# Performance work log

Measured on AMD Instinct MI355X. Metric: run time of the kernel, lower is better.

The kernel has to match this reference:

```python
import jax, jax.numpy as jnp
import numpy as np

N = 50000      # nodes
E = 320000     # edges
D_NODE = 256   # node feature size
D_EDGE = 128   # raw edge feature size
T_DIM = 64     # time encoder out_channels
H = 8          # heads (auto_num_heads(256) -> 8)
C = 32         # per-head dim = 256 // 8
D_E_IN = D_EDGE + T_DIM  # edge_dim into lin_edge


def setup_inputs() -> dict:
    key = jax.random.key(0)
    ks = jax.random.split(key, 16)
    s_n = 1.0 / np.sqrt(D_NODE)
    s_e = 1.0 / np.sqrt(D_E_IN)
    return {
        "edge_tuples": jax.random.randint(ks[0], (2, E), 0, N, dtype=jnp.int64)
        if jax.config.jax_enable_x64 else jax.random.randint(ks[0], (2, E), 0, N),
        "edge_feats": jax.random.normal(ks[1], (E, D_EDGE), jnp.float32),
        "edge_times_rel": jax.random.uniform(ks[2], (E,), jnp.float32) * 100.0,
        "node_feats": jax.random.normal(ks[3], (N, D_NODE), jnp.float32),
        # time encoder: Linear(1, T_DIM) followed by cos
        "w_time": jax.random.normal(ks[4], (T_DIM,), jnp.float32),
        "b_time": jax.random.normal(ks[5], (T_DIM,), jnp.float32),
        # TransformerConv linears (out = H*C = 256)
        "Wq": jax.random.normal(ks[6], (H * C, D_NODE), jnp.float32) * s_n,
        "bq": jnp.zeros((H * C,), jnp.float32),
        "Wk": jax.random.normal(ks[7], (H * C, D_NODE), jnp.float32) * s_n,
        "bk": jnp.zeros((H * C,), jnp.float32),
        "Wv": jax.random.normal(ks[8], (H * C, D_NODE), jnp.float32) * s_n,
        "bv": jnp.zeros((H * C,), jnp.float32),
        "We": jax.random.normal(ks[9], (H * C, D_E_IN), jnp.float32) * s_e,  # lin_edge, no bias
        "Ws": jax.random.normal(ks[10], (H * C, D_NODE), jnp.float32) * s_n,  # lin_skip
        "bs": jnp.zeros((H * C,), jnp.float32),
    }


def reference(edge_tuples, edge_feats, edge_times_rel, node_feats,
              w_time, b_time, Wq, bq, Wk, bk, Wv, bv, We, Ws, bs):
    n_nodes = node_feats.shape[0]
    n_edges = edge_tuples.shape[1]
    src, dst = edge_tuples[0], edge_tuples[1]

    # TGN time encoder: cos(t * w + b)  -> [E, T_DIM]
    tfeat = jnp.cos(edge_times_rel[:, None] * w_time[None, :] + b_time)
    e_attr = jnp.concatenate([tfeat, edge_feats], axis=1)  # [E, T_DIM + D_EDGE]

    # dense per-node projections, then gather per edge
    q = (node_feats @ Wq.T + bq)[dst].reshape(n_edges, H, C)
    k = (node_feats @ Wk.T + bk)[src].reshape(n_edges, H, C)
    v = (node_feats @ Wv.T + bv)[src].reshape(n_edges, H, C)
    ep = (e_attr @ We.T).reshape(n_edges, H, C)

    k = k + ep
    alpha = jnp.sum(q * k, axis=-1) / jnp.sqrt(jnp.asarray(C, q.dtype))  # [E, H]

    # segment softmax over edges grouped by destination node
    m = jax.ops.segment_max(alpha, dst, num_segments=n_nodes)  # [N, H]
    m = jnp.where(jnp.isfinite(m), m, 0.0)
    ea = jnp.exp(alpha - m[dst])
    denom = jax.ops.segment_sum(ea, dst, num_segments=n_nodes)
    a = ea / (denom[dst] + 1e-16)  # [E, H]

    # weighted scatter-aggregate of (value + edge) messages
    msg = a[:, :, None] * (v + ep)  # [E, H, C]
    out = jax.ops.segment_sum(msg, dst, num_segments=n_nodes).reshape(n_nodes, H * C)

    # root / skip connection
    out = out + node_feats @ Ws.T + bs
    return out
```

## Files before the change

kernel.cpp:

```cpp
#include <hip/hip_runtime.h>
#include <hip/hip_bf16.h>
#include <math.h>

#define NN 50000
#define NE 320000
#define SCAN_NBLK ((NN + 255) / 256)

typedef __attribute__((ext_vector_type(8))) short bf16x8;
typedef __attribute__((ext_vector_type(4))) float floatx4;
typedef __attribute__((ext_vector_type(4))) unsigned int uintx4;

static __device__ __forceinline__ unsigned pack2bf(float a, float b) {
    __hip_bfloat162 h = __float22bfloat162_rn(make_float2(a, b));
    return *reinterpret_cast<unsigned*>(&h);
}
static __device__ __forceinline__ unsigned short f2bf(float x) {
    __hip_bfloat16 h = __float2bfloat16(x);
    return *reinterpret_cast<unsigned short*>(&h);
}
static __device__ __forceinline__ float bf2f(unsigned short u) {
    return __uint_as_float(((unsigned)u) << 16);
}
static __device__ __forceinline__ float bflo(unsigned u) {
    return __uint_as_float(u << 16);
}
static __device__ __forceinline__ float bfhi(unsigned u) {
    return __uint_as_float(u & 0xffff0000u);
}
static __device__ __forceinline__ void gload_lds16(const void* g, void* l) {
    __builtin_amdgcn_global_load_lds(
        (const __attribute__((address_space(1))) void*)g,
        (__attribute__((address_space(3))) void*)l, 16, 0, 0);
}

__global__ __launch_bounds__(256)
void cvt_bf16_kernel(const float* __restrict__ in,
                     unsigned short* __restrict__ out, int n8)
{
    int t = blockIdx.x * 256 + threadIdx.x;
    if (t >= n8) return;
    const float4* p = (const float4*)in + (size_t)t * 2;
    float4 a = p[0], b = p[1];
    uint4 u;
    u.x = pack2bf(a.x, a.y); u.y = pack2bf(a.z, a.w);
    u.z = pack2bf(b.x, b.y); u.w = pack2bf(b.z, b.w);
    ((uint4*)out)[t] = u;
}

__global__ __launch_bounds__(256)
void node_gemm_kernel(const unsigned short* __restrict__ Xb,
                      const unsigned short* __restrict__ Wqb,
                      const unsigned short* __restrict__ Wkb,
                      const unsigned short* __restrict__ Wvb,
                      const unsigned short* __restrict__ Wsb,
                      const float* __restrict__ bq, const float* __restrict__ bk,
                      const float* __restrict__ bv, const float* __restrict__ bs,
                      unsigned short* __restrict__ qb,
                      unsigned short* __restrict__ kb,
                      unsigned short* __restrict__ vb,
                      float* __restrict__ outS)
{
    const int m0  = blockIdx.x * 128;
    const int ct  = blockIdx.y;
    const int mat = ct >> 1, half = ct & 1;
    const int colbase = half * 128;

    const unsigned short* __restrict__ W;
    const float* __restrict__ bias;
    switch (mat) {
        case 0:  W = Wqb; bias = bq; break;
        case 1:  W = Wkb; bias = bk; break;
        case 2:  W = Wvb; bias = bv; break;
        default: W = Wsb; bias = bs; break;
    }
    W += (size_t)colbase * 256;

    __shared__ __align__(16) unsigned char smem[32768];
    short* sA = (short*)smem;
    short* sB = (short*)(smem + 16384);

    const int tid  = threadIdx.x;
    const int lane = tid & 63;
    const int wave = tid >> 6;
    const int wm   = (wave & 1) * 64;
    const int wn   = (wave >> 1) * 64;
    const int lr   = lane & 15;
    const int lq   = lane >> 4;

    const int srow = tid >> 3;
    const int scol = (tid & 7) * 8;

    floatx4 acc[4][4];
    #pragma unroll
    for (int i = 0; i < 4; ++i)
        #pragma unroll
        for (int j = 0; j < 4; ++j)
            acc[i][j] = (floatx4){0.f, 0.f, 0.f, 0.f};

    for (int k0 = 0; k0 < 256; k0 += 64) {
        #pragma unroll
        for (int p = 0; p < 4; ++p) {
            int arow = m0 + p * 32 + srow;
            if (arow > NN - 1) arow = NN - 1;
            gload_lds16(Xb + (size_t)arow * 256 + k0 + scol,
                        (char*)sA + p * 4096 + wave * 1024);
            gload_lds16(W + (size_t)(p * 32 + srow) * 256 + k0 + scol,
                        (char*)sB + p * 4096 + wave * 1024);
        }
        __syncthreads();

        #pragma unroll
        for (int ks = 0; ks < 2; ++ks) {
            bf16x8 af[4], bfr[4];
            #pragma unroll
            for (int i = 0; i < 4; ++i)
                af[i] = *(const bf16x8*)&sA[(wm + i * 16 + lr) * 64 + ks * 32 + lq * 8];
            #pragma unroll
            for (int j = 0; j < 4; ++j)
                bfr[j] = *(const bf16x8*)&sB[(wn + j * 16 + lr) * 64 + ks * 32 + lq * 8];
            #pragma unroll
            for (int i = 0; i < 4; ++i)
                #pragma unroll
                for (int j = 0; j < 4; ++j)
                    acc[i][j] = __builtin_amdgcn_mfma_f32_16x16x32_bf16(
                        af[i], bfr[j], acc[i][j], 0, 0, 0);
        }
        __syncthreads();
    }

    if (mat < 3) {
        unsigned short* __restrict__ Cb = (mat == 0) ? qb : (mat == 1) ? kb : vb;
        unsigned short* sOut = (unsigned short*)smem;
        for (int ch = 0; ch < 4; ++ch) {
            __syncthreads();
            if ((ch >> 1) == (wave & 1)) {
                int ibase = (ch & 1) * 2;
                #pragma unroll
                for (int ii = 0; ii < 2; ++ii) {
                    int i = ibase + ii;
                    #pragma unroll
                    for (int j = 0; j < 4; ++j) {
                        int col = wn + j * 16 + lr;
                        float bb = bias[colbase + col];
                        #pragma unroll
                        for (int r = 0; r < 4; ++r) {
                            int rowc = ii * 16 + lq * 4 + r;
                            sOut[rowc * 136 + col] = f2bf(acc[i][j][r] + bb);
                        }
                    }
                }
            }
            __syncthreads();
            #pragma unroll
            for (int p = 0; p < 2; ++p) {
                int rowc = p * 16 + (tid >> 4);
                int off  = (tid & 15) * 8;
                int grow = m0 + ch * 32 + rowc;
                if (grow < NN) {
                    uint4 u = *(const uint4*)&sOut[rowc * 136 + off];
                    *(uint4*)&Cb[(size_t)grow * 256 + colbase + off] = u;
                }
            }
        }
    } else {
        float* sOutF = (float*)smem;
        for (int ch = 0; ch < 8; ++ch) {
            __syncthreads();
            if ((ch >> 2) == (wave & 1)) {
                int i = ch & 3;
                #pragma unroll
                for (int j = 0; j < 4; ++j) {
                    int col = wn + j * 16 + lr;
                    float bb = bias[colbase + col];
                    #pragma unroll
                    for (int r = 0; r < 4; ++r) {
                        int rowc = lq * 4 + r;
                        sOutF[rowc * 132 + col] = acc[i][j][r] + bb;
                    }
                }
            }
            __syncthreads();
            #pragma unroll
            for (int p = 0; p < 2; ++p) {
                int rowc = p * 8 + (tid >> 5);
                int off  = (tid & 31) * 4;
                int grow = m0 + ch * 16 + rowc;
                if (grow < NN) {
                    float4 f = *(const float4*)&sOutF[rowc * 132 + off];
                    *(float4*)&outS[(size_t)grow * 256 + colbase + off] = f;
                }
            }
        }
    }
}

__global__ __launch_bounds__(512)
void edge_gemm_kernel(const float* __restrict__ tvals,
                      const float* __restrict__ w_time,
                      const float* __restrict__ b_time,
                      const float* __restrict__ ef,
                      const unsigned short* __restrict__ Web,
                      unsigned short* __restrict__ epb)
{
    const int m0 = blockIdx.x * 128;

    __shared__ __align__(16) unsigned char smem[49152];
    short* sA = (short*)smem;
    short* sB = (short*)(smem + 16384);

    const int tid  = threadIdx.x;
    const int lane = tid & 63;
    const int wave = tid >> 6;
    const int wm   = (wave & 1) * 64;
    const int wn   = (wave >> 1) * 64;
    const int lr   = lane & 15;
    const int lq   = lane >> 4;

    floatx4 acc[4][4];
    #pragma unroll
    for (int i = 0; i < 4; ++i)
        #pragma unroll
        for (int j = 0; j < 4; ++j)
            acc[i][j] = (floatx4){0.f, 0.f, 0.f, 0.f};

    for (int k0 = 0; k0 < 192; k0 += 64) {
        #pragma unroll
        for (int p = 0; p < 4; ++p)
            gload_lds16(Web + (size_t)(p * 64 + (tid >> 3)) * 192 + k0 + (tid & 7) * 8,
                        (char*)sB + p * 8192 + wave * 1024);

        if (k0 == 0) {
            #pragma unroll
            for (int p = 0; p < 2; ++p) {
                int   row = p * 64 + (tid >> 3);
                float tvv = tvals[m0 + row];
                int   c0  = (tid & 7) * 8;
                float4 w0 = *(const float4*)(w_time + c0);
                float4 w1 = *(const float4*)(w_time + c0 + 4);
                float4 b0 = *(const float4*)(b_time + c0);
                float4 b1 = *(const float4*)(b_time + c0 + 4);
                uint4 u;
                u.x = pack2bf(cosf(fmaf(tvv, w0.x, b0.x)), cosf(fmaf(tvv, w0.y, b0.y)));
                u.y = pack2bf(cosf(fmaf(tvv, w0.z, b0.z)), cosf(fmaf(tvv, w0.w, b0.w)));
                u.z = pack2bf(cosf(fmaf(tvv, w1.x, b1.x)), cosf(fmaf(tvv, w1.y, b1.y)));
                u.w = pack2bf(cosf(fmaf(tvv, w1.z, b1.z)), cosf(fmaf(tvv, w1.w, b1.w)));
                *(uint4*)&sA[p * 4096 + tid * 8] = u;
            }
        } else {
            float4 f[4];
            #pragma unroll
            for (int p = 0; p < 2; ++p) {
                const float4* src = (const float4*)(ef
                    + (size_t)(m0 + p * 64 + (tid >> 3)) * 128 + (k0 - 64) + (tid & 7) * 8);
                f[2 * p]     = src[0];
                f[2 * p + 1] = src[1];
            }
            #pragma unroll
            for (int p = 0; p < 2; ++p) {
                uint4 u;
                u.x = pack2bf(f[2 * p].x,     f[2 * p].y);
                u.y = pack2bf(f[2 * p].z,     f[2 * p].w);
                u.z = pack2bf(f[2 * p + 1].x, f[2 * p + 1].y);
                u.w = pack2bf(f[2 * p + 1].z, f[2 * p + 1].w);
                *(uint4*)&sA[p * 4096 + tid * 8] = u;
            }
        }
        __syncthreads();

        #pragma unroll
        for (int ks = 0; ks < 2; ++ks) {
            bf16x8 af[4], bfr[4];
            #pragma unroll
            for (int i = 0; i < 4; ++i)
                af[i] = *(const bf16x8*)&sA[(wm + i * 16 + lr) * 64 + ks * 32 + lq * 8];
            #pragma unroll
            for (int j = 0; j < 4; ++j)
                bfr[j] = *(const bf16x8*)&sB[(wn + j * 16 + lr) * 64 + ks * 32 + lq * 8];
            #pragma unroll
            for (int i = 0; i < 4; ++i)
                #pragma unroll
                for (int j = 0; j < 4; ++j)
                    acc[i][j] = __builtin_amdgcn_mfma_f32_16x16x32_bf16(
                        af[i], bfr[j], acc[i][j], 0, 0, 0);
        }
        __syncthreads();
    }

    unsigned short* sOut = (unsigned short*)smem;
    for (int ch = 0; ch < 4; ++ch) {
        __syncthreads();
        if ((wave & 1) == (ch >> 1)) {
            int ibase = (ch & 1) * 2;
            #pragma unroll
            for (int ii = 0; ii < 2; ++ii) {
                int i = ibase + ii;
                #pragma unroll
                for (int j = 0; j < 4; ++j) {
                    int col = wn + j * 16 + lr;
                    #pragma unroll
                    for (int r = 0; r < 4; ++r) {
                        int rowc = ii * 16 + lq * 4 + r;
                        sOut[rowc * 264 + col] = f2bf(acc[i][j][r]);
                    }
                }
            }
        }
        __syncthreads();
        #pragma unroll
        for (int p = 0; p < 2; ++p) {
            int rl   = p * 16 + (tid >> 5);
            int off  = (tid & 31) * 8;
            int grow = m0 + ch * 32 + rl;
            uint4 u = *(const uint4*)&sOut[rl * 264 + off];
            *(uint4*)&epb[(size_t)grow * 256 + off] = u;
        }
    }
}

__global__ __launch_bounds__(256)
void deg_kernel(const int* __restrict__ et, int* __restrict__ deg)
{
    int e = blockIdx.x * 256 + threadIdx.x;
    if (e < NE) atomicAdd(&deg[et[NE + e]], 1);
}

__global__ __launch_bounds__(256)
void blocksum_kernel(const int* __restrict__ deg, int* __restrict__ bsum)
{
    int idx = blockIdx.x * 256 + threadIdx.x;
    int v = (idx < NN) ? deg[idx] : 0;
    #pragma unroll
    for (int off = 1; off < 64; off <<= 1) v += __shfl_xor(v, off);
    __shared__ int s[4];
    if ((threadIdx.x & 63) == 0) s[threadIdx.x >> 6] = v;
    __syncthreads();
    if (threadIdx.x == 0) bsum[blockIdx.x] = s[0] + s[1] + s[2] + s[3];
}

__global__ __launch_bounds__(256)
void bscan_kernel(int* __restrict__ bsum, int* __restrict__ rowstart)
{
    __shared__ int s[256];
    int t = threadIdx.x;
    int v = (t < SCAN_NBLK) ? bsum[t] : 0;
    s[t] = v;
    __syncthreads();
    #pragma unroll
    for (int off = 1; off < 256; off <<= 1) {
        int u = (t >= off) ? s[t - off] : 0;
        __syncthreads();
        s[t] += u;
        __syncthreads();
    }
    if (t < SCAN_NBLK) bsum[t] = (t == 0) ? 0 : s[t - 1];
    if (t == 0) rowstart[NN] = s[SCAN_NBLK - 1];
}

__global__ __launch_bounds__(256)
void chunkscan_kernel(const int* __restrict__ deg, const int* __restrict__ bsum,
                      int* __restrict__ rowstart, int* __restrict__ cursor)
{
    __shared__ int s[256];
    int t = threadIdx.x;
    int idx = blockIdx.x * 256 + t;
    int v = (idx < NN) ? deg[idx] : 0;
    s[t] = v;
    __syncthreads();
    #pragma unroll
    for (int off = 1; off < 256; off <<= 1) {
        int u = (t >= off) ? s[t - off] : 0;
        __syncthreads();
        s[t] += u;
        __syncthreads();
    }
    if (idx < NN) {
        int ex = bsum[blockIdx.x] + s[t] - v;
        rowstart[idx] = ex;
        cursor[idx]   = ex;
    }
}

__global__ __launch_bounds__(256)
void scatter_kernel(const int* __restrict__ et,
                    int* __restrict__ cursor,
                    int2* __restrict__ eslist)
{
    int e = blockIdx.x * 256 + threadIdx.x;
    if (e < NE) {
        int d   = et[NE + e];
        int pos = atomicAdd(&cursor[d], 1);
        eslist[pos] = make_int2(e, et[e]);
    }
}

static __device__ __forceinline__ void edge_proc(
    uint4 ku, uint4 vu, uintx4 eu, const float* q, float mask,
    float* a, float& accd)
{
    float pe0 = bflo(eu[0]), pe1 = bfhi(eu[0]);
    float pe2 = bflo(eu[1]), pe3 = bfhi(eu[1]);
    float pe4 = bflo(eu[2]), pe5 = bfhi(eu[2]);
    float pe6 = bflo(eu[3]), pe7 = bfhi(eu[3]);

    float part;
    part = q[0] * (bflo(ku.x) + pe0);
    part = fmaf(q[1], bfhi(ku.x) + pe1, part);
    part = fmaf(q[2], bflo(ku.y) + pe2, part);
    part = fmaf(q[3], bfhi(ku.y) + pe3, part);
    part = fmaf(q[4], bflo(ku.z) + pe4, part);
    part = fmaf(q[5], bfhi(ku.z) + pe5, part);
    part = fmaf(q[6], bflo(ku.w) + pe6, part);
    part = fmaf(q[7], bfhi(ku.w) + pe7, part);
    part += __shfl_xor(part, 1);
    part += __shfl_xor(part, 2);

    float ea = __expf(part * 0.17677669529663687f) * mask;

    a[0] = fmaf(ea, bflo(vu.x) + pe0, a[0]);
    a[1] = fmaf(ea, bfhi(vu.x) + pe1, a[1]);
    a[2] = fmaf(ea, bflo(vu.y) + pe2, a[2]);
    a[3] = fmaf(ea, bfhi(vu.y) + pe3, a[3]);
    a[4] = fmaf(ea, bflo(vu.z) + pe4, a[4]);
    a[5] = fmaf(ea, bfhi(vu.z) + pe5, a[5]);
    a[6] = fmaf(ea, bflo(vu.w) + pe6, a[6]);
    a[7] = fmaf(ea, bfhi(vu.w) + pe7, a[7]);
    accd += ea;
}

__global__ __launch_bounds__(256)
void fused_agg_kernel(const int2* __restrict__ eslist,
                      const int* __restrict__ rowstart,
                      const unsigned short* __restrict__ qb,
                      const unsigned short* __restrict__ kb,
                      const unsigned short* __restrict__ vb,
                      const unsigned short* __restrict__ epb,
                      float* __restrict__ out)
{
    const int n = blockIdx.x * 4 + (threadIdx.x >> 6);
    if (n >= NN) return;
    const int lane = threadIdx.x & 63;
    const int half = lane >> 5;
    const int co   = (lane & 31) * 8;

    uint4 qu = *(const uint4*)(qb + (size_t)n * 256 + co);
    float q[8] = { bflo(qu.x), bfhi(qu.x), bflo(qu.y), bfhi(qu.y),
                   bflo(qu.z), bfhi(qu.z), bflo(qu.w), bfhi(qu.w) };

    float a[8] = {0.f, 0.f, 0.f, 0.f, 0.f, 0.f, 0.f, 0.f};
    float accd = 0.f;

    const int s0 = rowstart[n];
    const int s1 = rowstart[n + 1];

    int i = s0;
    for (; i + 4 <= s1; i += 4) {
        const int2 pA = eslist[i + half];
        const int2 pB = eslist[i + 2 + half];
        uint4 kA = *(const uint4*)(kb + (size_t)pA.y * 256 + co);
        uint4 vA = *(const uint4*)(vb + (size_t)pA.y * 256 + co);
        uintx4 eA = __builtin_nontemporal_load(
                        (const uintx4*)(epb + (size_t)pA.x * 256 + co));
        uint4 kB = *(const uint4*)(kb + (size_t)pB.y * 256 + co);
        uint4 vB = *(const uint4*)(vb + (size_t)pB.y * 256 + co);
        uintx4 eB = __builtin_nontemporal_load(
                        (const uintx4*)(epb + (size_t)pB.x * 256 + co));

        edge_proc(kA, vA, eA, q, 1.f, a, accd);
        edge_proc(kB, vB, eB, q, 1.f, a, accd);
    }
    for (; i + 2 <= s1; i += 2) {
        const int2 pA = eslist[i + half];
        uint4 kA = *(const uint4*)(kb + (size_t)pA.y * 256 + co);
        uint4 vA = *(const uint4*)(vb + (size_t)pA.y * 256 + co);
        uintx4 eA = __builtin_nontemporal_load(
                        (const uintx4*)(epb + (size_t)pA.x * 256 + co));
        edge_proc(kA, vA, eA, q, 1.f, a, accd);
    }
    if (i < s1) {
        int idx = i + half;
        float mask = (idx < s1) ? 1.f : 0.f;
        if (idx >= s1) idx = s1 - 1;
        const int2 pA = eslist[idx];
        uint4 kA = *(const uint4*)(kb + (size_t)pA.y * 256 + co);
        uint4 vA = *(const uint4*)(vb + (size_t)pA.y * 256 + co);
        uintx4 eA = __builtin_nontemporal_load(
                        (const uintx4*)(epb + (size_t)pA.x * 256 + co));
        edge_proc(kA, vA, eA, q, mask, a, accd);
    }

    #pragma unroll
    for (int j = 0; j < 8; ++j) a[j] += __shfl_xor(a[j], 32);
    accd += __shfl_xor(accd, 32);

    if (half == 0) {
        const float inv = 1.f / (accd + 1e-16f);
        float* po = out + (size_t)n * 256 + co;
        float4 o0 = ((const float4*)po)[0];
        float4 o1 = ((const float4*)po)[1];
        o0.x = fmaf(a[0], inv, o0.x);
        o0.y = fmaf(a[1], inv, o0.y);
        o0.z = fmaf(a[2], inv, o0.z);
        o0.w = fmaf(a[3], inv, o0.w);
        o1.x = fmaf(a[4], inv, o1.x);
        o1.y = fmaf(a[5], inv, o1.y);
        o1.z = fmaf(a[6], inv, o1.z);
        o1.w = fmaf(a[7], inv, o1.w);
        ((float4*)po)[0] = o0;
        ((float4*)po)[1] = o1;
    }
}

extern "C" void kernel_launch(void* const* d_in, const int* in_sizes, int n_in,
                              void* d_out, int out_size, void* d_ws, size_t ws_size,
                              hipStream_t stream)
{
    const int*   et  = (const int*)  d_in[0];
    const float* ef  = (const float*)d_in[1];
    const float* tv  = (const float*)d_in[2];
    const float* nf  = (const float*)d_in[3];
    const float* w_t = (const float*)d_in[4];
    const float* b_t = (const float*)d_in[5];
    const float* Wq  = (const float*)d_in[6];
    const float* bq  = (const float*)d_in[7];
    const float* Wk  = (const float*)d_in[8];
    const float* bk  = (const float*)d_in[9];
    const float* Wv  = (const float*)d_in[10];
    const float* bv  = (const float*)d_in[11];
    const float* We  = (const float*)d_in[12];
    const float* Ws  = (const float*)d_in[13];
    const float* bs  = (const float*)d_in[14];
    float* out = (float*)d_out;

    unsigned short* qb  = (unsigned short*)d_ws;
    unsigned short* kb  = qb  + (size_t)NN * 256;
    unsigned short* vb  = kb  + (size_t)NN * 256;
    unsigned short* epb = vb  + (size_t)NN * 256;
    unsigned short* nfb = epb + (size_t)NE * 256;
    unsigned short* Wqb = nfb + (size_t)NN * 256;
    unsigned short* Wkb = Wqb + 65536;
    unsigned short* Wvb = Wkb + 65536;
    unsigned short* Wsb = Wvb + 65536;
    unsigned short* Web = Wsb + 65536;
    int* deg      = (int*)(Web + 49152);
    int* rowstart = deg + NN;
    int* cursor   = rowstart + NN + 1;
    int2* eslist  = (int2*)(cursor + NN);
    int* bsum     = (int*)(eslist + NE);
    size_t need   = (size_t)((char*)(bsum + SCAN_NBLK) - (char*)d_ws);
    if (ws_size < need) return;

    (void)hipMemsetAsync(deg, 0, (size_t)NN * sizeof(int), stream);

    cvt_bf16_kernel<<<(NN * 256 / 8 + 255) / 256, 256, 0, stream>>>(nf, nfb, NN * 256 / 8);
    cvt_bf16_kernel<<<32, 256, 0, stream>>>(Wq, Wqb, 8192);
    cvt_bf16_kernel<<<32, 256, 0, stream>>>(Wk, Wkb, 8192);
    cvt_bf16_kernel<<<32, 256, 0, stream>>>(Wv, Wvb, 8192);
    cvt_bf16_kernel<<<32, 256, 0, stream>>>(Ws, Wsb, 8192);
    cvt_bf16_kernel<<<24, 256, 0, stream>>>(We, Web, 6144);

    node_gemm_kernel<<<dim3((NN + 127) / 128, 8), 256, 0, stream>>>(
        nfb, Wqb, Wkb, Wvb, Wsb, bq, bk, bv, bs, qb, kb, vb, out);

    edge_gemm_kernel<<<NE / 128, 512, 0, stream>>>(
        tv, w_t, b_t, ef, Web, epb);

    deg_kernel<<<(NE + 255) / 256, 256, 0, stream>>>(et, deg);
    blocksum_kernel<<<SCAN_NBLK, 256, 0, stream>>>(deg, bsum);
    bscan_kernel<<<1, 256, 0, stream>>>(bsum, rowstart);
    chunkscan_kernel<<<SCAN_NBLK, 256, 0, stream>>>(deg, bsum, rowstart, cursor);
    scatter_kernel<<<(NE + 255) / 256, 256, 0, stream>>>(et, cursor, eslist);

    fused_agg_kernel<<<(NN + 3) / 4, 256, 0, stream>>>(
        eslist, rowstart, qb, kb, vb, epb, out);
}
```

Baseline: 579.0 us.

## Compute edge projections in destination-sorted order for sequential aggregation reads

```diff
diff --git a/kernel.cpp b/kernel.cpp
--- a/kernel.cpp
+++ b/kernel.cpp
@@ -200,6 +200,7 @@
                       const float* __restrict__ b_time,
                       const float* __restrict__ ef,
                       const unsigned short* __restrict__ Web,
+                      const int* __restrict__ elist,
                       unsigned short* __restrict__ epb)
 {
     const int m0 = blockIdx.x * 128;
@@ -215,6 +216,12 @@
     const int wn   = (wave >> 1) * 64;
     const int lr   = lane & 15;
     const int lq   = lane >> 4;
+    const int c8   = (tid & 7) * 8;
+
+    const int e0 = elist[m0 + (tid >> 3)];
+    const int e1 = elist[m0 + 64 + (tid >> 3)];
+    const float* __restrict__ efr0 = ef + (size_t)e0 * 128 + c8;
+    const float* __restrict__ efr1 = ef + (size_t)e1 * 128 + c8;
 
     floatx4 acc[4][4];
     #pragma unroll
@@ -223,68 +230,119 @@
         for (int j = 0; j < 4; ++j)
             acc[i][j] = (floatx4){0.f, 0.f, 0.f, 0.f};
 
-    for (int k0 = 0; k0 < 192; k0 += 64) {
-        #pragma unroll
-        for (int p = 0; p < 4; ++p)
-            gload_lds16(Web + (size_t)(p * 64 + (tid >> 3)) * 192 + k0 + (tid & 7) * 8,
-                        (char*)sB + p * 8192 + wave * 1024);
-
-        if (k0 == 0) {
-            #pragma unroll
-            for (int p = 0; p < 2; ++p) {
-                int   row = p * 64 + (tid >> 3);
-                float tvv = tvals[m0 + row];
-                int   c0  = (tid & 7) * 8;
-                float4 w0 = *(const float4*)(w_time + c0);
-                float4 w1 = *(const float4*)(w_time + c0 + 4);
-                float4 b0 = *(const float4*)(b_time + c0);
-                float4 b1 = *(const float4*)(b_time + c0 + 4);
-                uint4 u;
-                u.x = pack2bf(cosf(fmaf(tvv, w0.x, b0.x)), cosf(fmaf(tvv, w0.y, b0.y)));
-                u.y = pack2bf(cosf(fmaf(tvv, w0.z, b0.z)), cosf(fmaf(tvv, w0.w, b0.w)));
-                u.z = pack2bf(cosf(fmaf(tvv, w1.x, b1.x)), cosf(fmaf(tvv, w1.y, b1.y)));
-                u.w = pack2bf(cosf(fmaf(tvv, w1.z, b1.z)), cosf(fmaf(tvv, w1.w, b1.w)));
-                *(uint4*)&sA[p * 4096 + tid * 8] = u;
-            }
-        } else {
-            float4 f[4];
-            #pragma unroll
-            for (int p = 0; p < 2; ++p) {
-                const float4* src = (const float4*)(ef
-                    + (size_t)(m0 + p * 64 + (tid >> 3)) * 128 + (k0 - 64) + (tid & 7) * 8);
-                f[2 * p]     = src[0];
-                f[2 * p + 1] = src[1];
-            }
-            #pragma unroll
-            for (int p = 0; p < 2; ++p) {
-                uint4 u;
-                u.x = pack2bf(f[2 * p].x,     f[2 * p].y);
-                u.y = pack2bf(f[2 * p].z,     f[2 * p].w);
-                u.z = pack2bf(f[2 * p + 1].x, f[2 * p + 1].y);
-                u.w = pack2bf(f[2 * p + 1].z, f[2 * p + 1].w);
-                *(uint4*)&sA[p * 4096 + tid * 8] = u;
-            }
-        }
-        __syncthreads();
-
-        #pragma unroll
-        for (int ks = 0; ks < 2; ++ks) {
-            bf16x8 af[4], bfr[4];
-            #pragma unroll
-            for (int i = 0; i < 4; ++i)
-                af[i] = *(const bf16x8*)&sA[(wm + i * 16 + lr) * 64 + ks * 32 + lq * 8];
+    float4 f0 = ((const float4*)efr0)[0];
+    float4 f1 = ((const float4*)efr0)[1];
+    float4 f2 = ((const float4*)efr1)[0];
+    float4 f3 = ((const float4*)efr1)[1];
+
+    #pragma unroll
+    for (int p = 0; p < 4; ++p)
+        gload_lds16(Web + (size_t)(p * 64 + (tid >> 3)) * 192 + 0 + c8,
+                    (char*)sB + p * 8192 + wave * 1024);
+    {
+        float4 w0 = *(const float4*)(w_time + c8);
+        float4 w1 = *(const float4*)(w_time + c8 + 4);
+        float4 b0 = *(const float4*)(b_time + c8);
+        float4 b1 = *(const float4*)(b_time + c8 + 4);
+        float tv0 = tvals[e0], tv1 = tvals[e1];
+        uint4 u;
+        u.x = pack2bf(cosf(fmaf(tv0, w0.x, b0.x)), cosf(fmaf(tv0, w0.y, b0.y)));
+        u.y = pack2bf(cosf(fmaf(tv0, w0.z, b0.z)), cosf(fmaf(tv0, w0.w, b0.w)));
+        u.z = pack2bf(cosf(fmaf(tv0, w1.x, b1.x)), cosf(fmaf(tv0, w1.y, b1.y)));
+        u.w = pack2bf(cosf(fmaf(tv0, w1.z, b1.z)), cosf(fmaf(tv0, w1.w, b1.w)));
+        *(uint4*)&sA[tid * 8] = u;
+        u.x = pack2bf(cosf(fmaf(tv1, w0.x, b0.x)), cosf(fmaf(tv1, w0.y, b0.y)));
+        u.y = pack2bf(cosf(fmaf(tv1, w0.z, b0.z)), cosf(fmaf(tv1, w0.w, b0.w)));
+        u.z = pack2bf(cosf(fmaf(tv1, w1.x, b1.x)), cosf(fmaf(tv1, w1.y, b1.y)));
+        u.w = pack2bf(cosf(fmaf(tv1, w1.z, b1.z)), cosf(fmaf(tv1, w1.w, b1.w)));
+        *(uint4*)&sA[4096 + tid * 8] = u;
+    }
+    __syncthreads();
+    #pragma unroll
+    for (int ks = 0; ks < 2; ++ks) {
+        bf16x8 af[4], bfr[4];
+        #pragma unroll
+        for (int i = 0; i < 4; ++i)
+            af[i] = *(const bf16x8*)&sA[(wm + i * 16 + lr) * 64 + ks * 32 + lq * 8];
+        #pragma unroll
+        for (int j = 0; j < 4; ++j)
+            bfr[j] = *(const bf16x8*)&sB[(wn + j * 16 + lr) * 64 + ks * 32 + lq * 8];
+        #pragma unroll
+        for (int i = 0; i < 4; ++i)
             #pragma unroll
             for (int j = 0; j < 4; ++j)
-                bfr[j] = *(const bf16x8*)&sB[(wn + j * 16 + lr) * 64 + ks * 32 + lq * 8];
-            #pragma unroll
-            for (int i = 0; i < 4; ++i)
-                #pragma unroll
-                for (int j = 0; j < 4; ++j)
-                    acc[i][j] = __builtin_amdgcn_mfma_f32_16x16x32_bf16(
-                        af[i], bfr[j], acc[i][j], 0, 0, 0);
-        }
-        __syncthreads();
-    }
+                acc[i][j] = __builtin_amdgcn_mfma_f32_16x16x32_bf16(
+                    af[i], bfr[j], acc[i][j], 0, 0, 0);
+    }
+    __syncthreads();
+
+    {
+        uint4 u;
+        u.x = pack2bf(f0.x, f0.y); u.y = pack2bf(f0.z, f0.w);
+        u.z = pack2bf(f1.x, f1.y); u.w = pack2bf(f1.z, f1.w);
+        *(uint4*)&sA[tid * 8] = u;
+        u.x = pack2bf(f2.x, f2.y); u.y = pack2bf(f2.z, f2.w);
+        u.z = pack2bf(f3.x, f3.y); u.w = pack2bf(f3.z, f3.w);
+        *(uint4*)&sA[4096 + tid * 8] = u;
+    }
+    f0 = ((const float4*)(efr0 + 64))[0];
+    f1 = ((const float4*)(efr0 + 64))[1];
+    f2 = ((const float4*)(efr1 + 64))[0];
+    f3 = ((const float4*)(efr1 + 64))[1];
+    #pragma unroll
+    for (int p = 0; p < 4; ++p)
+        gload_lds16(Web + (size_t)(p * 64 + (tid >> 3)) * 192 + 64 + c8,
+                    (char*)sB + p * 8192 + wave * 1024);
+    __syncthreads();
+    #pragma unroll
+    for (int ks = 0; ks < 2; ++ks) {
+        bf16x8 af[4], bfr[4];
+        #pragma unroll
+        for (int i = 0; i < 4; ++i)
+            af[i] = *(const bf16x8*)&sA[(wm + i * 16 + lr) * 64 + ks * 32 + lq * 8];
+        #pragma unroll
+        for (int j = 0; j < 4; ++j)
+            bfr[j] = *(const bf16x8*)&sB[(wn + j * 16 + lr) * 64 + ks * 32 + lq * 8];
+        #pragma unroll
+        for (int i = 0; i < 4; ++i)
+            #pragma unroll
+            for (int j = 0; j < 4; ++j)
+                acc[i][j] = __builtin_amdgcn_mfma_f32_16x16x32_bf16(
+                    af[i], bfr[j], acc[i][j], 0, 0, 0);
+    }
+    __syncthreads();
+
+    {
+        uint4 u;
+        u.x = pack2bf(f0.x, f0.y); u.y = pack2bf(f0.z, f0.w);
+        u.z = pack2bf(f1.x, f1.y); u.w = pack2bf(f1.z, f1.w);
+        *(uint4*)&sA[tid * 8] = u;
+        u.x = pack2bf(f2.x, f2.y); u.y = pack2bf(f2.z, f2.w);
+        u.z = pack2bf(f3.x, f3.y); u.w = pack2bf(f3.z, f3.w);
+        *(uint4*)&sA[4096 + tid * 8] = u;
+    }
+    #pragma unroll
+    for (int p = 0; p < 4; ++p)
+        gload_lds16(Web + (size_t)(p * 64 + (tid >> 3)) * 192 + 128 + c8,
+                    (char*)sB + p * 8192 + wave * 1024);
+    __syncthreads();
+    #pragma unroll
+    for (int ks = 0; ks < 2; ++ks) {
+        bf16x8 af[4], bfr[4];
+        #pragma unroll
+        for (int i = 0; i < 4; ++i)
+            af[i] = *(const bf16x8*)&sA[(wm + i * 16 + lr) * 64 + ks * 32 + lq * 8];
+        #pragma unroll
+        for (int j = 0; j < 4; ++j)
+            bfr[j] = *(const bf16x8*)&sB[(wn + j * 16 + lr) * 64 + ks * 32 + lq * 8];
+        #pragma unroll
+        for (int i = 0; i < 4; ++i)
+            #pragma unroll
+            for (int j = 0; j < 4; ++j)
+                acc[i][j] = __builtin_amdgcn_mfma_f32_16x16x32_bf16(
+                    af[i], bfr[j], acc[i][j], 0, 0, 0);
+    }
+    __syncthreads();
 
     unsigned short* sOut = (unsigned short*)smem;
     for (int ch = 0; ch < 4; ++ch) {
@@ -383,13 +441,14 @@
 __global__ __launch_bounds__(256)
 void scatter_kernel(const int* __restrict__ et,
                     int* __restrict__ cursor,
-                    int2* __restrict__ eslist)
+                    int* __restrict__ elist, int* __restrict__ slist)
 {
     int e = blockIdx.x * 256 + threadIdx.x;
     if (e < NE) {
         int d   = et[NE + e];
         int pos = atomicAdd(&cursor[d], 1);
-        eslist[pos] = make_int2(e, et[e]);
+        elist[pos] = e;
+        slist[pos] = et[e];
     }
 }
 
@@ -428,7 +487,7 @@
 }
 
 __global__ __launch_bounds__(256)
-void fused_agg_kernel(const int2* __restrict__ eslist,
+void fused_agg_kernel(const int* __restrict__ slist,
                       const int* __restrict__ rowstart,
                       const unsigned short* __restrict__ qb,
                       const unsigned short* __restrict__ kb,
@@ -454,37 +513,39 @@
 
     int i = s0;
     for (; i + 4 <= s1; i += 4) {
-        const int2 pA = eslist[i + half];
-        const int2 pB = eslist[i + 2 + half];
-        uint4 kA = *(const uint4*)(kb + (size_t)pA.y * 256 + co);
-        uint4 vA = *(const uint4*)(vb + (size_t)pA.y * 256 + co);
+        const int iA = i + half, iB = i + 2 + half;
+        const int srcA = slist[iA];
+        const int srcB = slist[iB];
+        uint4 kA = *(const uint4*)(kb + (size_t)srcA * 256 + co);
+        uint4 vA = *(const uint4*)(vb + (size_t)srcA * 256 + co);
         uintx4 eA = __builtin_nontemporal_load(
-                        (const uintx4*)(epb + (size_t)pA.x * 256 + co));
-        uint4 kB = *(const uint4*)(kb + (size_t)pB.y * 256 + co);
-        uint4 vB = *(const uint4*)(vb + (size_t)pB.y * 256 + co);
+                        (const uintx4*)(epb + (size_t)iA * 256 + co));
+        uint4 kB = *(const uint4*)(kb + (size_t)srcB * 256 + co);
+        uint4 vB = *(const uint4*)(vb + (size_t)srcB * 256 + co);
         uintx4 eB = __builtin_nontemporal_load(
-                        (const uintx4*)(epb + (size_t)pB.x * 256 + co));
+                        (const uintx4*)(epb + (size_t)iB * 256 + co));
 
         edge_proc(kA, vA, eA, q, 1.f, a, accd);
         edge_proc(kB, vB, eB, q, 1.f, a, accd);
     }
     for (; i + 2 <= s1; i += 2) {
-        const int2 pA = eslist[i + half];
-        uint4 kA = *(const uint4*)(kb + (size_t)pA.y * 256 + co);
-        uint4 vA = *(const uint4*)(vb + (size_t)pA.y * 256 + co);
+        const int iA = i + half;
+        const int srcA = slist[iA];
+        uint4 kA = *(const uint4*)(kb + (size_t)srcA * 256 + co);
+        uint4 vA = *(const uint4*)(vb + (size_t)srcA * 256 + co);
         uintx4 eA = __builtin_nontemporal_load(
-                        (const uintx4*)(epb + (size_t)pA.x * 256 + co));
+                        (const uintx4*)(epb + (size_t)iA * 256 + co));
         edge_proc(kA, vA, eA, q, 1.f, a, accd);
     }
     if (i < s1) {
         int idx = i + half;
         float mask = (idx < s1) ? 1.f : 0.f;
         if (idx >= s1) idx = s1 - 1;
-        const int2 pA = eslist[idx];
-        uint4 kA = *(const uint4*)(kb + (size_t)pA.y * 256 + co);
-        uint4 vA = *(const uint4*)(vb + (size_t)pA.y * 256 + co);
+        const int srcA = slist[idx];
+        uint4 kA = *(const uint4*)(kb + (size_t)srcA * 256 + co);
+        uint4 vA = *(const uint4*)(vb + (size_t)srcA * 256 + co);
         uintx4 eA = __builtin_nontemporal_load(
-                        (const uintx4*)(epb + (size_t)pA.x * 256 + co));
+                        (const uintx4*)(epb + (size_t)idx * 256 + co));
         edge_proc(kA, vA, eA, q, mask, a, accd);
     }
 
@@ -544,12 +605,19 @@
     int* deg      = (int*)(Web + 49152);
     int* rowstart = deg + NN;
     int* cursor   = rowstart + NN + 1;
-    int2* eslist  = (int2*)(cursor + NN);
-    int* bsum     = (int*)(eslist + NE);
+    int* elist    = cursor + NN;
+    int* slist    = elist + NE;
+    int* bsum     = slist + NE;
     size_t need   = (size_t)((char*)(bsum + SCAN_NBLK) - (char*)d_ws);
     if (ws_size < need) return;
 
     (void)hipMemsetAsync(deg, 0, (size_t)NN * sizeof(int), stream);
+
+    deg_kernel<<<(NE + 255) / 256, 256, 0, stream>>>(et, deg);
+    blocksum_kernel<<<SCAN_NBLK, 256, 0, stream>>>(deg, bsum);
+    bscan_kernel<<<1, 256, 0, stream>>>(bsum, rowstart);
+    chunkscan_kernel<<<SCAN_NBLK, 256, 0, stream>>>(deg, bsum, rowstart, cursor);
+    scatter_kernel<<<(NE + 255) / 256, 256, 0, stream>>>(et, cursor, elist, slist);
 
     cvt_bf16_kernel<<<(NN * 256 / 8 + 255) / 256, 256, 0, stream>>>(nf, nfb, NN * 256 / 8);
     cvt_bf16_kernel<<<32, 256, 0, stream>>>(Wq, Wqb, 8192);
@@ -562,14 +630,8 @@
         nfb, Wqb, Wkb, Wvb, Wsb, bq, bk, bv, bs, qb, kb, vb, out);
 
     edge_gemm_kernel<<<NE / 128, 512, 0, stream>>>(
-        tv, w_t, b_t, ef, Web, epb);
-
-    deg_kernel<<<(NE + 255) / 256, 256, 0, stream>>>(et, deg);
-    blocksum_kernel<<<SCAN_NBLK, 256, 0, stream>>>(deg, bsum);
-    bscan_kernel<<<1, 256, 0, stream>>>(bsum, rowstart);
-    chunkscan_kernel<<<SCAN_NBLK, 256, 0, stream>>>(deg, bsum, rowstart, cursor);
-    scatter_kernel<<<(NE + 255) / 256, 256, 0, stream>>>(et, cursor, eslist);
+        tv, w_t, b_t, ef, Web, elist, epb);
 
     fused_agg_kernel<<<(NN + 3) / 4, 256, 0, stream>>>(
-        eslist, rowstart, qb, kb, vb, epb, out);
-}
+        slist, rowstart, qb, kb, vb, epb, out);
+}
```

Result: faster. 551.4 us (-4.8%).
